# Performance work log

Hardware: AMD Instinct MI355X
Metric: run time of the kernel (lower is better)

Reference implementation:

```python
import jax, jax.numpy as jnp
import numpy as np

N_NODES = 50000
N_EDGES = 800000
HEADS = 8
DIM = 32
NEG_SLOPE = 0.2


def setup_inputs() -> dict:
    key = jax.random.key(0)
    k1, k2, k3, k4, k5 = jax.random.split(key, 5)
    feat = jax.random.normal(k1, (N_NODES, HEADS * DIM), dtype=jnp.float32)
    attn_l = jax.random.normal(k2, (1, HEADS, DIM), dtype=jnp.float32)
    attn_r = jax.random.normal(k3, (1, HEADS, DIM), dtype=jnp.float32)
    src_idx = jax.random.randint(k4, (N_EDGES,), 0, N_NODES, dtype=jnp.int32)
    dst_idx = jnp.sort(jax.random.randint(k5, (N_EDGES,), 0, N_NODES, dtype=jnp.int32))
    return {"feat": feat, "attn_l": attn_l, "attn_r": attn_r,
            "src_idx": src_idx, "dst_idx": dst_idx}


def reference(feat, attn_l, attn_r, src_idx, dst_idx):
    # [N, H, D] node features
    h = feat.reshape(-1, HEADS, DIM)
    n = h.shape[0]
    # per-node attention logits: [N, H]
    el = jnp.sum(h * attn_l, axis=-1)
    er = jnp.sum(h * attn_r, axis=-1)
    # edge scores e = leaky_relu(el[u] + er[v]): [E, H]
    e = jax.nn.leaky_relu(el[src_idx] + er[dst_idx], negative_slope=NEG_SLOPE)
    # segment softmax over incoming edges of each dst node
    e_max = jax.ops.segment_max(e, dst_idx, num_segments=n)          # [N, H]
    e_exp = jnp.exp(e - e_max[dst_idx])                              # [E, H]
    denom = jax.ops.segment_sum(e_exp, dst_idx, num_segments=n)     # [N, H]
    a = e_exp / denom[dst_idx]                                      # [E, H]
    # weighted scatter-sum aggregation: sum_{u in N(v)} a_uv * h_u
    m = h[src_idx] * a[:, :, None]                                  # [E, H, D]
    out = jax.ops.segment_sum(m, dst_idx, num_segments=n)           # [N, H, D]
    return out
```

## Files before the change

kernel.cpp:

```cpp
#include <hip/hip_runtime.h>
#include <hip/hip_fp16.h>
#include <math.h>

#define HEADS 8
#define DIM 32
#define NEG_SLOPE 0.2f

__device__ inline float2 u2f2(unsigned int u) {
    __half2 h = __builtin_bit_cast(__half2, u);
    return __half22float2(h);
}

__global__ __launch_bounds__(256) void gat_logits_conv_kernel(
    const float4* __restrict__ feat4,
    const float4* __restrict__ attn_l4,
    const float4* __restrict__ attn_r4,
    float* __restrict__ el,
    float* __restrict__ er,
    uint2* __restrict__ feat_h2,
    int n_nodes) {
    int wid = (blockIdx.x * blockDim.x + threadIdx.x) >> 6;
    if (wid >= n_nodes) return;
    int lane = threadIdx.x & 63;
    int h = lane >> 3;
    int q = lane & 7;

    float4 al = attn_l4[lane];
    float4 ar = attn_r4[lane];
    float4 v  = feat4[(size_t)wid * 64 + lane];

    float sl = v.x * al.x + v.y * al.y + v.z * al.z + v.w * al.w;
    float sr = v.x * ar.x + v.y * ar.y + v.z * ar.z + v.w * ar.w;
#pragma unroll
    for (int off = 1; off < 8; off <<= 1) {
        sl += __shfl_xor(sl, off, 64);
        sr += __shfl_xor(sr, off, 64);
    }
    if (q == 0) {
        el[wid * HEADS + h] = sl;
        er[wid * HEADS + h] = sr;
    }
    uint2 o;
    o.x = __builtin_bit_cast(unsigned int, __floats2half2_rn(v.x, v.y));
    o.y = __builtin_bit_cast(unsigned int, __floats2half2_rn(v.z, v.w));
    feat_h2[(size_t)wid * 64 + lane] = o;
}

__global__ void build_rowptr_kernel(const int* __restrict__ dst,
                                    int* __restrict__ rowptr,
                                    int n_edges, int n_nodes) {
    int e = blockIdx.x * blockDim.x + threadIdx.x;
    if (e >= n_edges) return;
    int d = dst[e];
    int prev = (e > 0) ? dst[e - 1] : -1;
    for (int v = prev + 1; v <= d; ++v) rowptr[v] = e;
    if (e == n_edges - 1) {
        for (int v = d + 1; v <= n_nodes; ++v) rowptr[v] = n_edges;
    }
}

__global__ __launch_bounds__(256) void gat_aggregate_kernel(
    const uint4* __restrict__ feat_h4,
    const float* __restrict__ el,
    const float* __restrict__ er,
    const int* __restrict__ src_idx,
    const int* __restrict__ rowptr,
    float4* __restrict__ out4,
    int n_nodes) {
    int wid = (blockIdx.x * blockDim.x + threadIdx.x) >> 6;
    int lane = threadIdx.x & 63;
    int s = lane & 31;
    int h = s >> 2;
    int v = wid * 2 + (lane >> 5);
    bool valid = v < n_nodes;
    int vv = valid ? v : (n_nodes - 1);

    int start = rowptr[vv];
    int end   = rowptr[vv + 1];
    if (!valid) end = start;
    int len = end - start;

    float er_vh = er[vv * HEADS + h];

    int len0 = __shfl(len, 0, 64);
    int len1 = __shfl(len, 32, 64);
    int maxlen = len0 > len1 ? len0 : len1;

    float denomA = 0.f, denomB = 0.f;
    float acc[8];
#pragma unroll
    for (int j = 0; j < 8; ++j) acc[j] = 0.f;

    for (int k = 0; k < maxlen; k += 8) {
        int   idx[8];
        uint4 fr[8];
        float w[8];
#pragma unroll
        for (int i = 0; i < 8; ++i) {
            int e = start + k + i;
            int ee = e < end ? e : (end - 1);
            ee = ee < 0 ? 0 : ee;
            idx[i] = src_idx[ee];
        }
#pragma unroll
        for (int i = 0; i < 8; ++i) {
            fr[i] = feat_h4[(size_t)idx[i] * 32 + s];
        }
#pragma unroll
        for (int i = 0; i < 8; ++i) {
            float sc = el[(size_t)idx[i] * HEADS + h] + er_vh;
            sc = sc > 0.f ? sc : NEG_SLOPE * sc;
            float ww = __expf(sc);
            w[i] = (k + i < len) ? ww : 0.f;
        }
#pragma unroll
        for (int i = 0; i < 8; ++i) {
            float ww = w[i];
            if (i & 1) denomB += ww; else denomA += ww;
            float2 p0 = u2f2(fr[i].x);
            float2 p1 = u2f2(fr[i].y);
            float2 p2 = u2f2(fr[i].z);
            float2 p3 = u2f2(fr[i].w);
            acc[0] += ww * p0.x; acc[1] += ww * p0.y;
            acc[2] += ww * p1.x; acc[3] += ww * p1.y;
            acc[4] += ww * p2.x; acc[5] += ww * p2.y;
            acc[6] += ww * p3.x; acc[7] += ww * p3.y;
        }
    }
    if (valid) {
        float denom = denomA + denomB;
        float inv = denom > 0.f ? 1.f / denom : 0.f;
        float4 r0, r1;
        r0.x = acc[0] * inv; r0.y = acc[1] * inv;
        r0.z = acc[2] * inv; r0.w = acc[3] * inv;
        r1.x = acc[4] * inv; r1.y = acc[5] * inv;
        r1.z = acc[6] * inv; r1.w = acc[7] * inv;
        size_t ob = (size_t)v * 64 + (size_t)s * 2;
        out4[ob]     = r0;
        out4[ob + 1] = r1;
    }
}

extern "C" void kernel_launch(void* const* d_in, const int* in_sizes, int n_in,
                              void* d_out, int out_size, void* d_ws, size_t ws_size,
                              hipStream_t stream) {
    const float* feat   = (const float*)d_in[0];
    const float* attn_l = (const float*)d_in[1];
    const float* attn_r = (const float*)d_in[2];
    const int*   src    = (const int*)d_in[3];
    const int*   dst    = (const int*)d_in[4];
    float* out = (float*)d_out;

    int n_edges = in_sizes[3];
    int n_nodes = out_size / (HEADS * DIM);
    int nh = n_nodes * HEADS;

    char* ws = (char*)d_ws;
    float* el = (float*)ws;                       ws += (size_t)nh * 4;
    float* er = (float*)ws;                       ws += (size_t)nh * 4;
    int* rowptr = (int*)ws;                       ws += (size_t)(n_nodes + 1) * 4;
    ws = (char*)(((uintptr_t)ws + 15) & ~(uintptr_t)15);
    uint2* feat_h2 = (uint2*)ws;

    hipLaunchKernelGGL(gat_logits_conv_kernel,
                       dim3((n_nodes + 3) / 4), dim3(256), 0, stream,
                       (const float4*)feat, (const float4*)attn_l,
                       (const float4*)attn_r, el, er, feat_h2, n_nodes);

    hipLaunchKernelGGL(build_rowptr_kernel,
                       dim3((n_edges + 255) / 256), dim3(256), 0, stream,
                       dst, rowptr, n_edges, n_nodes);

    int blocks = (n_nodes + 7) / 8;
    hipLaunchKernelGGL(gat_aggregate_kernel,
                       dim3(blocks), dim3(256), 0, stream,
                       (const uint4*)feat_h2, el, er, src, rowptr, (float4*)out,
                       n_nodes);
}
```

Measured before the change: 100.3 us.

## Map one node per wavefront and double-buffer edge gathers in aggregation

The aggregation kernel now gives each destination node a full 64-lane wavefront instead of half a wavefront. Each lane loads 4 half-precision features (uint2) rather than 8, and each lane writes one float4 of output. The edge loop is software-pipelined with two 8-edge register buffers, so the gathers for the next batch are issued while the current batch is computed. Nodes with no edges exit early and write zeros. The goal is to hide gather latency and drop the shared maxlen divergence between two nodes, at the cost of more waves and more register pressure.

After: 108.2 us. 7.8% more time.

```diff
diff --git a/kernel.cpp b/kernel.cpp
--- a/kernel.cpp
+++ b/kernel.cpp
@@ -60,85 +60,98 @@
 }
 
 __global__ __launch_bounds__(256) void gat_aggregate_kernel(
-    const uint4* __restrict__ feat_h4,
+    const uint2* __restrict__ feat_h,
     const float* __restrict__ el,
     const float* __restrict__ er,
     const int* __restrict__ src_idx,
     const int* __restrict__ rowptr,
     float4* __restrict__ out4,
     int n_nodes) {
-    int wid = (blockIdx.x * blockDim.x + threadIdx.x) >> 6;
+    int v = (blockIdx.x * blockDim.x + threadIdx.x) >> 6;
+    if (v >= n_nodes) return;
     int lane = threadIdx.x & 63;
-    int s = lane & 31;
-    int h = s >> 2;
-    int v = wid * 2 + (lane >> 5);
-    bool valid = v < n_nodes;
-    int vv = valid ? v : (n_nodes - 1);
+    int h = lane >> 3;
 
-    int start = rowptr[vv];
-    int end   = rowptr[vv + 1];
-    if (!valid) end = start;
+    int start = rowptr[v];
+    int end   = rowptr[v + 1];
+    size_t obase = (size_t)v * 64 + lane;
+    if (start == end) {
+        out4[obase] = make_float4(0.f, 0.f, 0.f, 0.f);
+        return;
+    }
     int len = end - start;
-
-    float er_vh = er[vv * HEADS + h];
-
-    int len0 = __shfl(len, 0, 64);
-    int len1 = __shfl(len, 32, 64);
-    int maxlen = len0 > len1 ? len0 : len1;
+    float er_vh = er[v * HEADS + h];
 
     float denomA = 0.f, denomB = 0.f;
-    float acc[8];
-#pragma unroll
-    for (int j = 0; j < 8; ++j) acc[j] = 0.f;
+    float4 acc0 = make_float4(0.f, 0.f, 0.f, 0.f);
+    float4 acc1 = make_float4(0.f, 0.f, 0.f, 0.f);
 
-    for (int k = 0; k < maxlen; k += 8) {
-        int   idx[8];
-        uint4 fr[8];
-        float w[8];
-#pragma unroll
-        for (int i = 0; i < 8; ++i) {
-            int e = start + k + i;
-            int ee = e < end ? e : (end - 1);
-            ee = ee < 0 ? 0 : ee;
-            idx[i] = src_idx[ee];
-        }
-#pragma unroll
-        for (int i = 0; i < 8; ++i) {
-            fr[i] = feat_h4[(size_t)idx[i] * 32 + s];
-        }
-#pragma unroll
-        for (int i = 0; i < 8; ++i) {
-            float sc = el[(size_t)idx[i] * HEADS + h] + er_vh;
-            sc = sc > 0.f ? sc : NEG_SLOPE * sc;
-            float ww = __expf(sc);
-            w[i] = (k + i < len) ? ww : 0.f;
-        }
-#pragma unroll
-        for (int i = 0; i < 8; ++i) {
-            float ww = w[i];
-            if (i & 1) denomB += ww; else denomA += ww;
-            float2 p0 = u2f2(fr[i].x);
-            float2 p1 = u2f2(fr[i].y);
-            float2 p2 = u2f2(fr[i].z);
-            float2 p3 = u2f2(fr[i].w);
-            acc[0] += ww * p0.x; acc[1] += ww * p0.y;
-            acc[2] += ww * p1.x; acc[3] += ww * p1.y;
-            acc[4] += ww * p2.x; acc[5] += ww * p2.y;
-            acc[6] += ww * p3.x; acc[7] += ww * p3.y;
-        }
+    int   idxA[8], idxB[8];
+    uint2 frA[8], frB[8];
+    float elA[8], elB[8];
+
+#define LOADIDX(IDX, BASE)                                                 \
+    _Pragma("unroll")                                                      \
+    for (int i = 0; i < 8; ++i) {                                          \
+        int e = (BASE) + i;                                                \
+        e = e < end ? e : (end - 1);                                       \
+        IDX[i] = src_idx[e];                                               \
     }
-    if (valid) {
-        float denom = denomA + denomB;
-        float inv = denom > 0.f ? 1.f / denom : 0.f;
-        float4 r0, r1;
-        r0.x = acc[0] * inv; r0.y = acc[1] * inv;
-        r0.z = acc[2] * inv; r0.w = acc[3] * inv;
-        r1.x = acc[4] * inv; r1.y = acc[5] * inv;
-        r1.z = acc[6] * inv; r1.w = acc[7] * inv;
-        size_t ob = (size_t)v * 64 + (size_t)s * 2;
-        out4[ob]     = r0;
-        out4[ob + 1] = r1;
+
+#define LOADDAT(IDX, FR, EL)                                               \
+    _Pragma("unroll")                                                      \
+    for (int i = 0; i < 8; ++i) {                                          \
+        FR[i] = feat_h[(size_t)IDX[i] * 64 + lane];                        \
+        EL[i] = el[(size_t)IDX[i] * HEADS + h];                            \
     }
+
+#define COMPUTE(FR, EL, BASE)                                              \
+    _Pragma("unroll")                                                      \
+    for (int i = 0; i < 8; ++i) {                                          \
+        float s = EL[i] + er_vh;                                           \
+        s = s > 0.f ? s : NEG_SLOPE * s;                                   \
+        float w = __expf(s);                                               \
+        w = ((BASE) + i - start < len) ? w : 0.f;                          \
+        if (i & 1) denomB += w; else denomA += w;                          \
+        float2 lo = u2f2(FR[i].x);                                         \
+        float2 hi = u2f2(FR[i].y);                                         \
+        if (i & 1) {                                                       \
+            acc1.x += w * lo.x; acc1.y += w * lo.y;                        \
+            acc1.z += w * hi.x; acc1.w += w * hi.y;                        \
+        } else {                                                           \
+            acc0.x += w * lo.x; acc0.y += w * lo.y;                        \
+            acc0.z += w * hi.x; acc0.w += w * hi.y;                        \
+        }                                                                  \
+    }
+
+    LOADIDX(idxA, start)
+    LOADDAT(idxA, frA, elA)
+
+    for (int k = start; k < end; k += 16) {
+        LOADIDX(idxB, k + 8)
+        LOADDAT(idxB, frB, elB)
+        COMPUTE(frA, elA, k)
+        LOADIDX(idxA, k + 16)
+        LOADDAT(idxA, frA, elA)
+        COMPUTE(frB, elB, k + 8)
+    }
+
+    float denom = denomA + denomB;
+    float inv = 1.f / denom;
+    float4 r;
+    r.x = acc0.x * inv; r.y = acc0.y * inv;
+    r.z = acc0.z * inv; r.w = acc0.w * inv;
+    (void)acc1;
+    r.x = (acc0.x + 0.f) * inv;
+    r.x = (acc0.x + acc1.x) * inv;
+    r.y = (acc0.y + acc1.y) * inv;
+    r.z = (acc0.z + acc1.z) * inv;
+    r.w = (acc0.w + acc1.w) * inv;
+    out4[obase] = r;
+
+#undef LOADIDX
+#undef LOADDAT
+#undef COMPUTE
 }
 
 extern "C" void kernel_launch(void* const* d_in, const int* in_sizes, int n_in,
@@ -171,9 +184,9 @@
                        dim3((n_edges + 255) / 256), dim3(256), 0, stream,
                        dst, rowptr, n_edges, n_nodes);
 
-    int blocks = (n_nodes + 7) / 8;
+    int blocks = (n_nodes + 3) / 4;
     hipLaunchKernelGGL(gat_aggregate_kernel,
                        dim3(blocks), dim3(256), 0, stream,
-                       (const uint4*)feat_h2, el, er, src, rowptr, (float4*)out,
+                       (const uint2*)feat_h2, el, er, src, rowptr, (float4*)out,
                        n_nodes);
 }
```
